# Performance work log

Measured on AMD Instinct MI355X. Metric: run time of the kernel, lower is better.

Reference implementation:

```python
import jax, jax.numpy as jnp
import numpy as np

N, E, C, H, L, G, K, NC = 50000, 500000, 256, 128, 4, 64, 8, 2
EPS_MSG = 1e-7  # GENConv message eps
EPS_BN = 1e-5   # BatchNorm eps


def setup_inputs() -> dict:
    key = jax.random.key(0)
    ks = jax.random.split(key, 32)
    def nrm(k, shape, scale):
        return jax.random.normal(k, shape, dtype=jnp.float32) * scale
    sC = 1.0 / np.sqrt(C).astype(np.float32)
    sH = 1.0 / np.sqrt(H).astype(np.float32)
    s2H = 1.0 / np.sqrt(2 * H).astype(np.float32)
    return dict(
        x=nrm(ks[0], (N, C), 1.0),
        edge_index=jax.random.randint(ks[1], (2, E), 0, N, dtype=jnp.int32),
        edge_attr=jax.random.uniform(ks[2], (E, 1), dtype=jnp.float32),
        batch=jnp.sort(jax.random.randint(ks[3], (N,), 0, G, dtype=jnp.int32)),
        clinical=nrm(ks[4], (G, K), 1.0),
        lin_src_w=nrm(ks[5], (C, H), sC), lin_src_b=nrm(ks[6], (H,), 0.01),
        lin_dst_w=nrm(ks[7], (C, H), sC), lin_dst_b=nrm(ks[8], (H,), 0.01),
        edge_w=nrm(ks[9], (L, 1, H), 1.0), edge_b=nrm(ks[10], (L, H), 0.01),
        t=0.1 + 0.01 * jax.random.normal(ks[11], (L,), dtype=jnp.float32),
        mlp_w1=nrm(ks[12], (L, H, 2 * H), sH), mlp_b1=nrm(ks[13], (L, 2 * H), 0.01),
        mlp_bn_g=1.0 + nrm(ks[14], (L, 2 * H), 0.1), mlp_bn_b=nrm(ks[15], (L, 2 * H), 0.1),
        mlp_bn_m=nrm(ks[16], (L, 2 * H), 0.1),
        mlp_bn_v=1.0 + jax.random.uniform(ks[17], (L, 2 * H), dtype=jnp.float32),
        mlp_w2=nrm(ks[18], (L, 2 * H, H), s2H), mlp_b2=nrm(ks[19], (L, H), 0.01),
        norm_g=1.0 + nrm(ks[20], (L, H), 0.1), norm_b=nrm(ks[21], (L, H), 0.1),
        norm_m=nrm(ks[22], (L, H), 0.1),
        norm_v=1.0 + jax.random.uniform(ks[23], (L, H), dtype=jnp.float32),
        cls_w=nrm(ks[24], (H + K, NC), 1.0 / np.sqrt(H + K).astype(np.float32)),
        cls_b=nrm(ks[25], (NC,), 0.01),
    )


def _bn(h, g, b, m, v):
    # eval-mode BatchNorm with running stats
    return g * (h - m) * jax.lax.rsqrt(v + EPS_BN) + b


def reference(x, edge_index, edge_attr, batch, clinical,
              lin_src_w, lin_src_b, lin_dst_w, lin_dst_b,
              edge_w, edge_b, t,
              mlp_w1, mlp_b1, mlp_bn_g, mlp_bn_b, mlp_bn_m, mlp_bn_v,
              mlp_w2, mlp_b2, norm_g, norm_b, norm_m, norm_v,
              cls_w, cls_b):
    n = x.shape[0]
    g_count = clinical.shape[0]
    src, dst = edge_index[0], edge_index[1]
    n_layers = t.shape[0]

    def genconv(xs, xd, l):
        # xs: source features feeding messages [N,H]; xd: dst skip features [N,H]
        e = edge_attr @ edge_w[l] + edge_b[l]               # [E,H]
        msg = jax.nn.relu(xs[src] + e) + EPS_MSG            # [E,H]
        z = msg * t[l]
        zmax = jax.ops.segment_max(z, dst, num_segments=n)  # [N,H]
        zmax = jnp.where(jnp.isfinite(zmax), zmax, 0.0)
        ez = jnp.exp(z - zmax[dst])
        denom = jax.ops.segment_sum(ez, dst, num_segments=n)
        agg = jax.ops.segment_sum(msg * ez, dst, num_segments=n) / jnp.maximum(denom, 1e-16)
        out = agg + xd
        # internal MLP [H, 2H, H]: Linear -> BN -> ReLU -> Linear
        hmid = jax.nn.relu(_bn(out @ mlp_w1[l] + mlp_b1[l],
                               mlp_bn_g[l], mlp_bn_b[l], mlp_bn_m[l], mlp_bn_v[l]))
        return hmid @ mlp_w2[l] + mlp_b2[l]

    # layer 0: conv only (per DeepGCN.forward); lin_src / lin_dst project C -> H
    xs0 = x @ lin_src_w + lin_src_b
    xd0 = x @ lin_dst_w + lin_dst_b
    h = genconv(xs0, xd0, 0)

    # layers 1..L-1: res+ block (norm -> act -> conv, residual add); dropout = identity (eval)
    for l in range(1, n_layers):
        r = jax.nn.relu(_bn(h, norm_g[l], norm_b[l], norm_m[l], norm_v[l]))
        h = h + genconv(r, r, l)

    # final norm/act from layer 0
    h = jax.nn.relu(_bn(h, norm_g[0], norm_b[0], norm_m[0], norm_v[0]))

    # global mean pool over graphs
    cnt = jax.ops.segment_sum(jnp.ones((n,), h.dtype), batch, num_segments=g_count)
    pooled = jax.ops.segment_sum(h, batch, num_segments=g_count) / jnp.maximum(cnt, 1.0)[:, None]

    z = jnp.concatenate([pooled, clinical], axis=1)
    return z @ cls_w + cls_b  # [G, num_classes]; squeeze is a no-op for G>1, NC=2
```

## Files before the change

### kernel.cpp

```cpp
#include <hip/hip_runtime.h>
#include <math.h>

#define Nn 50000
#define MPAD 50048
#define Ee 500000
#define Cc 256
#define Hh 128
#define Ll 4
#define Gg 64
#define Kk 8
#define NCc 2

#define NB 196

typedef __attribute__((ext_vector_type(8))) short short8;
typedef __attribute__((ext_vector_type(4))) float f32x4;
typedef __attribute__((ext_vector_type(2))) float f32x2;

__device__ __forceinline__ unsigned short f2bf(float f) {
    union { float f; unsigned int u; } v;
    v.f = f;
    unsigned int u = v.u;
    return (unsigned short)((u + 0x7FFFu + ((u >> 16) & 1u)) >> 16);
}
__device__ __forceinline__ float bf2f(unsigned short s) {
    union { float f; unsigned int u; } v;
    v.u = ((unsigned int)s) << 16;
    return v.f;
}
__device__ __forceinline__ float bf2f_lo(unsigned int u) {
    union { float f; unsigned int u; } v;
    v.u = u << 16;
    return v.f;
}
__device__ __forceinline__ float bf2f_hi(unsigned int u) {
    union { float f; unsigned int u; } v;
    v.u = u & 0xffff0000u;
    return v.f;
}


__global__ void hist_kernel(const int* __restrict__ dst, int* __restrict__ deg) {
    int e = blockIdx.x * 256 + threadIdx.x;
    if (e < Ee) atomicAdd(&deg[dst[e]], 1);
}

__global__ __launch_bounds__(256) void bsum_kernel(const int* __restrict__ deg,
                                                   int* __restrict__ bsum) {
    __shared__ int ws[4];
    int t = threadIdx.x;
    int i = blockIdx.x * 256 + t;
    int v = (i < Nn) ? deg[i] : 0;
#pragma unroll
    for (int o = 32; o; o >>= 1) v += __shfl_down(v, o, 64);
    if ((t & 63) == 0) ws[t >> 6] = v;
    __syncthreads();
    if (t == 0) bsum[blockIdx.x] = ws[0] + ws[1] + ws[2] + ws[3];
}

__global__ __launch_bounds__(256) void bscan_kernel(const int* __restrict__ bsum,
                                                    int* __restrict__ boff,
                                                    int* __restrict__ off) {
    __shared__ int sc[256];
    int t = threadIdx.x;
    int v = (t < NB) ? bsum[t] : 0;
    sc[t] = v;
    __syncthreads();
    for (int o = 1; o < 256; o <<= 1) {
        int u = (t >= o) ? sc[t - o] : 0;
        __syncthreads();
        sc[t] += u;
        __syncthreads();
    }
    if (t < NB) boff[t] = sc[t] - v;
    if (t == NB - 1) off[Nn] = sc[t];
}

__global__ __launch_bounds__(256) void offsets_kernel(const int* __restrict__ deg,
                                                      const int* __restrict__ boff,
                                                      int* __restrict__ off,
                                                      int* __restrict__ pos) {
    __shared__ int sc[256];
    int t = threadIdx.x;
    int i = blockIdx.x * 256 + t;
    int v = (i < Nn) ? deg[i] : 0;
    sc[t] = v;
    __syncthreads();
    for (int o = 1; o < 256; o <<= 1) {
        int u = (t >= o) ? sc[t - o] : 0;
        __syncthreads();
        sc[t] += u;
        __syncthreads();
    }
    int excl = sc[t] - v + boff[blockIdx.x];
    if (i < Nn) {
        off[i] = excl;
        pos[i] = excl;
    }
}

__global__ void scatter_kernel(const int* __restrict__ src, const int* __restrict__ dst,
                               const float* __restrict__ attr, int* __restrict__ pos,
                               int2* __restrict__ sedge) {
    int e = blockIdx.x * 256 + threadIdx.x;
    if (e < Ee) {
        int d = dst[e];
        int p = atomicAdd(&pos[d], 1);
        sedge[p] = make_int2(src[e], __float_as_int(attr[e]));
    }
}


__global__ void wconv_kernel(const float* __restrict__ lin_src_w,
                             const float* __restrict__ lin_dst_w,
                             const float* __restrict__ mlp_w1,
                             const float* __restrict__ mlp_w2,
                             unsigned short* __restrict__ wt) {
    int idx = blockIdx.x * 256 + threadIdx.x;
    if (idx >= 327680) return;
    float val;
    if (idx < 65536) {
        int n = idx >> 8, k = idx & 255;
        val = (n < 128) ? lin_src_w[k * 128 + n] : lin_dst_w[k * 128 + (n - 128)];
    } else if (idx < 196608) {
        int r = idx - 65536;
        int l = r >> 15, e = r & 32767;
        int n = e >> 7, k = e & 127;
        val = mlp_w1[(size_t)l * 32768 + k * 256 + n];
    } else {
        int r = idx - 196608;
        int l = r >> 15, e = r & 32767;
        int n = e >> 8, k = e & 255;
        val = mlp_w2[(size_t)l * 32768 + k * 128 + n];
    }
    wt[idx] = f2bf(val);
}


__global__ __launch_bounds__(256) void xconv_kernel(const float* __restrict__ x,
                                                    unsigned short* __restrict__ xbf) {
    int idx = blockIdx.x * 256 + threadIdx.x;
    if (idx >= (Nn * Cc) / 8) return;
    const float4* p = (const float4*)(x) + (size_t)idx * 2;
    float4 v0 = p[0], v1 = p[1];
    unsigned short t[8];
    t[0] = f2bf(v0.x); t[1] = f2bf(v0.y); t[2] = f2bf(v0.z); t[3] = f2bf(v0.w);
    t[4] = f2bf(v1.x); t[5] = f2bf(v1.y); t[6] = f2bf(v1.z); t[7] = f2bf(v1.w);
    *(short8*)(xbf + (size_t)idx * 8) = *(short8*)t;
}

#define GLOAD16(gp, lp)                                                                       \
    __builtin_amdgcn_global_load_lds(                                                         \
        (const __attribute__((address_space(1))) unsigned int*)(gp),                          \
        (__attribute__((address_space(3))) unsigned int*)(lp), 16, 0, 0)


__global__ __launch_bounds__(256) void proj_kernel(
    const unsigned short* __restrict__ A, const unsigned short* __restrict__ Bt,
    const float* __restrict__ bias, const float* __restrict__ bias2,
    unsigned short* __restrict__ Cout) {
    __shared__ __align__(16) unsigned short SH[24576];
    int tid = threadIdx.x;
    int wave = tid >> 6, lane = tid & 63;
    int wr = wave >> 1, wc = wave & 1;
    int lrow = lane & 15, quad = lane >> 4;
    int m0 = blockIdx.y * 128, n0 = blockIdx.x * 128;
    const int K = 256;

    const unsigned short* ag0 = A + (size_t)(m0 + (tid >> 2)) * K + (tid & 3) * 8;
    const unsigned short* ag1 = A + (size_t)(m0 + 64 + (tid >> 2)) * K + (tid & 3) * 8;
    const unsigned short* bg0 = Bt + (size_t)(n0 + (tid >> 2)) * K + (tid & 3) * 8;
    const unsigned short* bg1 = Bt + (size_t)(n0 + 64 + (tid >> 2)) * K + (tid & 3) * 8;

    f32x4 acc[4][4];
#pragma unroll
    for (int i = 0; i < 4; i++)
#pragma unroll
        for (int j = 0; j < 4; j++) acc[i][j] = (f32x4){0.f, 0.f, 0.f, 0.f};

    auto stage = [&](int buf, int koff) {
        GLOAD16(ag0 + koff, SH + buf * 4096 + wave * 512);
        GLOAD16(ag1 + koff, SH + buf * 4096 + 2048 + wave * 512);
        GLOAD16(bg0 + koff, SH + 12288 + buf * 4096 + wave * 512);
        GLOAD16(bg1 + koff, SH + 12288 + buf * 4096 + 2048 + wave * 512);
    };

    const int ntiles = 8;
    stage(0, 0);
    stage(1, 32);
    for (int t = 0; t < ntiles; ++t) {
        if (t + 1 < ntiles) {
            asm volatile("s_waitcnt vmcnt(4)\n\ts_barrier" ::: "memory");
        } else {
            asm volatile("s_waitcnt vmcnt(0)\n\ts_barrier" ::: "memory");
        }
        if (t + 2 < ntiles) stage((t + 2) % 3, (t + 2) * 32);
        int cur = t % 3;
        const unsigned short* As = SH + cur * 4096;
        const unsigned short* Bs = SH + 12288 + cur * 4096;
        short8 af[4], bfr[4];
#pragma unroll
        for (int mt = 0; mt < 4; mt++)
            af[mt] = *(const short8*)&As[(wr * 64 + mt * 16 + lrow) * 32 + quad * 8];
#pragma unroll
        for (int nf = 0; nf < 4; nf++)
            bfr[nf] = *(const short8*)&Bs[(wc * 64 + nf * 16 + lrow) * 32 + quad * 8];
#pragma unroll
        for (int mt = 0; mt < 4; mt++)
#pragma unroll
            for (int nf = 0; nf < 4; nf++)
                acc[mt][nf] = __builtin_amdgcn_mfma_f32_16x16x32_bf16(af[mt], bfr[nf],
                                                                     acc[mt][nf], 0, 0, 0);
    }

    __syncthreads();
    unsigned short* Cl = SH;
#pragma unroll
    for (int nf = 0; nf < 4; nf++) {
        int gc = n0 + wc * 64 + nf * 16 + lrow;
        float bs = (gc >= 128) ? bias2[gc - 128] : bias[gc];
        int col = wc * 64 + nf * 16 + lrow;
#pragma unroll
        for (int mt = 0; mt < 4; mt++)
#pragma unroll
            for (int r = 0; r < 4; r++)
                Cl[(wr * 64 + mt * 16 + quad * 4 + r) * 128 + col] = f2bf(acc[mt][nf][r] + bs);
    }
    __syncthreads();
#pragma unroll
    for (int p = 0; p < 8; p++) {
        int vid = p * 256 + tid;
        int row = vid >> 4, cg = (vid & 15) * 8;
        short8 v = *(const short8*)&Cl[row * 128 + cg];
        *(short8*)(Cout + (size_t)(m0 + row) * 256 + n0 + cg) = v;
    }
}


__global__ __launch_bounds__(256) void mlp_kernel(
    const unsigned short* __restrict__ A,
    const unsigned short* __restrict__ W1,
    const unsigned short* __restrict__ W2,
    const float* __restrict__ b1, const float* __restrict__ bn_g,
    const float* __restrict__ bn_b, const float* __restrict__ bn_m,
    const float* __restrict__ bn_v, const float* __restrict__ b2,
    const float* __restrict__ pn_g, const float* __restrict__ pn_b,
    const float* __restrict__ pn_m, const float* __restrict__ pn_v,
    float* __restrict__ hbuf, unsigned short* __restrict__ rbuf, int rmw) {
    __shared__ __align__(16) unsigned short S[20480];
    __shared__ __align__(16) unsigned short Hm[64 * 264];

    int tid = threadIdx.x;
    int wave = tid >> 6, lane = tid & 63;
    int lrow = lane & 15, quad = lane >> 4;
    int m0 = blockIdx.x * 64;

    const unsigned short* ag = A + (size_t)(m0 + (tid >> 2)) * 128 + (tid & 3) * 8;
    const unsigned short* bg = W1 + (size_t)(tid >> 2) * 128 + (tid & 3) * 8;

    f32x4 acc1[4][4];
#pragma unroll
    for (int i = 0; i < 4; i++)
#pragma unroll
        for (int j = 0; j < 4; j++) acc1[i][j] = (f32x4){0.f, 0.f, 0.f, 0.f};

    auto stage1 = [&](int buf, int k0) {
        GLOAD16(ag + k0, S + buf * 2048 + wave * 512);
#pragma unroll
        for (int c = 0; c < 4; c++)
            GLOAD16(bg + (size_t)c * 64 * 128 + k0,
                    S + 4096 + buf * 8192 + c * 2048 + wave * 512);
    };

    stage1(0, 0);
    __syncthreads();
    for (int t = 0; t < 4; ++t) {
        if (t + 1 < 4) stage1((t + 1) & 1, (t + 1) * 32);
        int cur = t & 1;
        const unsigned short* A1s = S + cur * 2048;
        const unsigned short* B1s = S + 4096 + cur * 8192;
        short8 af[4], bfr[4];
#pragma unroll
        for (int mt = 0; mt < 4; mt++)
            af[mt] = *(const short8*)&A1s[(mt * 16 + lrow) * 32 + quad * 8];
#pragma unroll
        for (int nf = 0; nf < 4; nf++)
            bfr[nf] = *(const short8*)&B1s[(wave * 64 + nf * 16 + lrow) * 32 + quad * 8];
#pragma unroll
        for (int mt = 0; mt < 4; mt++)
#pragma unroll
            for (int nf = 0; nf < 4; nf++)
                acc1[mt][nf] = __builtin_amdgcn_mfma_f32_16x16x32_bf16(af[mt], bfr[nf],
                                                                      acc1[mt][nf], 0, 0, 0);
        __syncthreads();
    }

#pragma unroll
    for (int nf = 0; nf < 4; nf++) {
        int gc = wave * 64 + nf * 16 + lrow;
        float bs = b1[gc];
        float g = bn_g[gc], bb = bn_b[gc], mm = bn_m[gc];
        float inv = rsqrtf(bn_v[gc] + 1e-5f);
#pragma unroll
        for (int mt = 0; mt < 4; mt++)
#pragma unroll
            for (int r = 0; r < 4; r++) {
                float v = acc1[mt][nf][r] + bs;
                v = fmaxf(g * (v - mm) * inv + bb, 0.f);
                Hm[(mt * 16 + quad * 4 + r) * 264 + gc] = f2bf(v);
            }
    }
    __syncthreads();

    const unsigned short* b2g0 = W2 + (size_t)(tid >> 2) * 256 + (tid & 3) * 8;
    const unsigned short* b2g1 = W2 + (size_t)(64 + (tid >> 2)) * 256 + (tid & 3) * 8;

    f32x4 acc2[4][2];
#pragma unroll
    for (int i = 0; i < 4; i++)
#pragma unroll
        for (int j = 0; j < 2; j++) acc2[i][j] = (f32x4){0.f, 0.f, 0.f, 0.f};

    auto stage2 = [&](int buf, int k0) {
        GLOAD16(b2g0 + k0, S + buf * 4096 + wave * 512);
        GLOAD16(b2g1 + k0, S + buf * 4096 + 2048 + wave * 512);
    };

    stage2(0, 0);
    __syncthreads();
    for (int t = 0; t < 8; ++t) {
        if (t + 1 < 8) stage2((t + 1) & 1, (t + 1) * 32);
        int cur = t & 1;
        const unsigned short* B2s = S + cur * 4096;
        short8 af[4], bfr[2];
#pragma unroll
        for (int mt = 0; mt < 4; mt++)
            af[mt] = *(const short8*)&Hm[(mt * 16 + lrow) * 264 + t * 32 + quad * 8];
#pragma unroll
        for (int nf = 0; nf < 2; nf++)
            bfr[nf] = *(const short8*)&B2s[(wave * 32 + nf * 16 + lrow) * 32 + quad * 8];
#pragma unroll
        for (int mt = 0; mt < 4; mt++)
#pragma unroll
            for (int nf = 0; nf < 2; nf++)
                acc2[mt][nf] = __builtin_amdgcn_mfma_f32_16x16x32_bf16(af[mt], bfr[nf],
                                                                      acc2[mt][nf], 0, 0, 0);
        __syncthreads();
    }

    float* C2 = (float*)S;
#pragma unroll
    for (int nf = 0; nf < 2; nf++) {
        int gc = wave * 32 + nf * 16 + lrow;
        float bs = b2[gc];
#pragma unroll
        for (int mt = 0; mt < 4; mt++)
#pragma unroll
            for (int r = 0; r < 4; r++)
                C2[(mt * 16 + quad * 4 + r) * 128 + gc] = acc2[mt][nf][r] + bs;
    }
    __syncthreads();
#pragma unroll
    for (int p = 0; p < 8; p++) {
        int vid = p * 256 + tid;
        int row = vid >> 5, c4 = (vid & 31) * 4;
        f32x4 v = *(const f32x4*)&C2[row * 128 + c4];
        float* hp = hbuf + (size_t)(m0 + row) * 128 + c4;
        if (rmw) v += *(const f32x4*)hp;
        *(f32x4*)hp = v;
        if (pn_g) {
            f32x4 pg = *(const f32x4*)&pn_g[c4];
            f32x4 pb = *(const f32x4*)&pn_b[c4];
            f32x4 pm = *(const f32x4*)&pn_m[c4];
            f32x4 pv = *(const f32x4*)&pn_v[c4];
            float r0 = fmaxf(pg[0] * (v[0] - pm[0]) * rsqrtf(pv[0] + 1e-5f) + pb[0], 0.f);
            float r1 = fmaxf(pg[1] * (v[1] - pm[1]) * rsqrtf(pv[1] + 1e-5f) + pb[1], 0.f);
            float r2 = fmaxf(pg[2] * (v[2] - pm[2]) * rsqrtf(pv[2] + 1e-5f) + pb[2], 0.f);
            float r3 = fmaxf(pg[3] * (v[3] - pm[3]) * rsqrtf(pv[3] + 1e-5f) + pb[3], 0.f);
            unsigned int w0 = (unsigned int)f2bf(r0) | ((unsigned int)f2bf(r1) << 16);
            unsigned int w1 = (unsigned int)f2bf(r2) | ((unsigned int)f2bf(r3) << 16);
            uint2 pk = make_uint2(w0, w1);
            *(uint2*)(rbuf + (size_t)(m0 + row) * 128 + c4) = pk;
        }
    }
}


template <int XSS>
__global__ __launch_bounds__(256) void agg_kernel(
    const unsigned short* __restrict__ xs,
    const unsigned short* __restrict__ xd, int xds,
    const int2* __restrict__ sedge, const int* __restrict__ off,
    const float* __restrict__ ew, const float* __restrict__ eb,
    const float* __restrict__ tptr, unsigned short* __restrict__ outb) {
    int wave = threadIdx.x >> 6;
    int lane = threadIdx.x & 63;
    int d = blockIdx.x * 4 + wave;
    int s0 = __builtin_amdgcn_readfirstlane(off[d]);
    int s1 = __builtin_amdgcn_readfirstlane(off[d + 1]);
    int f0 = lane * 2;
    unsigned int ud = *(const unsigned int*)(xd + (size_t)d * xds + f0);
    f32x2 wv = *(const f32x2*)(ew + f0);
    f32x2 bv = *(const f32x2*)(eb + f0);
    float c = tptr[0] * 1.44269504088896f;
    const f32x2 zz = {0.f, 0.f};
    f32x2 den = {0.f, 0.f}, num = {0.f, 0.f};

#define EDGE2(u, av)                                                \
    {                                                               \
        f32x2 xv = {bf2f_lo(u), bf2f_hi(u)};                        \
        f32x2 m = __builtin_elementwise_max(xv + bv + (av)*wv, zz); \
        f32x2 e;                                                    \
        e.x = __builtin_amdgcn_exp2f(m.x * c);                      \
        e.y = __builtin_amdgcn_exp2f(m.y * c);                      \
        den += e;                                                   \
        num += m * e;                                               \
    }
#define EDGE2M(u, av, mk)                                           \
    {                                                               \
        f32x2 xv = {bf2f_lo(u), bf2f_hi(u)};                        \
        f32x2 m = __builtin_elementwise_max(xv + bv + (av)*wv, zz); \
        f32x2 e;                                                    \
        e.x = __builtin_amdgcn_exp2f(m.x * c) * (mk);               \
        e.y = __builtin_amdgcn_exp2f(m.y * c) * (mk);               \
        den += e;                                                   \
        num += m * e;                                               \
    }

    int j = s0;
    for (; j + 8 <= s1; j += 8) {
        int4 q0 = *(const int4*)(sedge + j);
        int4 q1 = *(const int4*)(sedge + j + 2);
        int4 q2 = *(const int4*)(sedge + j + 4);
        int4 q3 = *(const int4*)(sedge + j + 6);
        int i0 = __builtin_amdgcn_readfirstlane(q0.x);
        int i1 = __builtin_amdgcn_readfirstlane(q0.z);
        int i2 = __builtin_amdgcn_readfirstlane(q1.x);
        int i3 = __builtin_amdgcn_readfirstlane(q1.z);
        int i4 = __builtin_amdgcn_readfirstlane(q2.x);
        int i5 = __builtin_amdgcn_readfirstlane(q2.z);
        int i6 = __builtin_amdgcn_readfirstlane(q3.x);
        int i7 = __builtin_amdgcn_readfirstlane(q3.z);
        float a0 = __int_as_float(__builtin_amdgcn_readfirstlane(q0.y));
        float a1 = __int_as_float(__builtin_amdgcn_readfirstlane(q0.w));
        float a2 = __int_as_float(__builtin_amdgcn_readfirstlane(q1.y));
        float a3 = __int_as_float(__builtin_amdgcn_readfirstlane(q1.w));
        float a4 = __int_as_float(__builtin_amdgcn_readfirstlane(q2.y));
        float a5 = __int_as_float(__builtin_amdgcn_readfirstlane(q2.w));
        float a6 = __int_as_float(__builtin_amdgcn_readfirstlane(q3.y));
        float a7 = __int_as_float(__builtin_amdgcn_readfirstlane(q3.w));
        unsigned int u0 = *(const unsigned int*)(xs + (size_t)i0 * XSS + f0);
        unsigned int u1 = *(const unsigned int*)(xs + (size_t)i1 * XSS + f0);
        unsigned int u2 = *(const unsigned int*)(xs + (size_t)i2 * XSS + f0);
        unsigned int u3 = *(const unsigned int*)(xs + (size_t)i3 * XSS + f0);
        unsigned int u4 = *(const unsigned int*)(xs + (size_t)i4 * XSS + f0);
        unsigned int u5 = *(const unsigned int*)(xs + (size_t)i5 * XSS + f0);
        unsigned int u6 = *(const unsigned int*)(xs + (size_t)i6 * XSS + f0);
        unsigned int u7 = *(const unsigned int*)(xs + (size_t)i7 * XSS + f0);
        EDGE2(u0, a0)
        EDGE2(u1, a1)
        EDGE2(u2, a2)
        EDGE2(u3, a3)
        EDGE2(u4, a4)
        EDGE2(u5, a5)
        EDGE2(u6, a6)
        EDGE2(u7, a7)
    }
    if (j < s1) {
        int last = s1 - 1;
        int ii[8];
        float aa[8], mk[8];
#pragma unroll
        for (int k = 0; k < 8; k++) {
            int jj = j + k;
            int cl = (jj < s1) ? jj : last;
            int2 p = sedge[cl];
            ii[k] = __builtin_amdgcn_readfirstlane(p.x);
            aa[k] = __int_as_float(__builtin_amdgcn_readfirstlane(p.y));
            mk[k] = (jj < s1) ? 1.f : 0.f;
        }
        unsigned int uu[8];
#pragma unroll
        for (int k = 0; k < 8; k++)
            uu[k] = *(const unsigned int*)(xs + (size_t)ii[k] * XSS + f0);
#pragma unroll
        for (int k = 0; k < 8; k++) EDGE2M(uu[k], aa[k], mk[k])
    }
#undef EDGE2
#undef EDGE2M
    float a0 = (s1 > s0) ? (num.x / den.x + 1e-7f) : 0.f;
    float a1 = (s1 > s0) ? (num.y / den.y + 1e-7f) : 0.f;
    unsigned int lo = f2bf(a0 + bf2f_lo(ud));
    unsigned int hi = f2bf(a1 + bf2f_hi(ud));
    *(unsigned int*)(outb + (size_t)d * Hh + f0) = lo | (hi << 16);
}


#define PCHUNK 100

__global__ __launch_bounds__(128) void pool_kernel(
    const float* __restrict__ h, const int* __restrict__ batch,
    const float* __restrict__ g, const float* __restrict__ b,
    const float* __restrict__ m, const float* __restrict__ v,
    float* __restrict__ pooled, float* __restrict__ cnt) {
    int hh = threadIdx.x;
    int i0 = blockIdx.x * PCHUNK;
    int i1 = min(i0 + PCHUNK, Nn);
    if (i0 >= Nn) return;
    float gg = g[hh], bb = b[hh], mm = m[hh], inv = rsqrtf(v[hh] + 1e-5f);
    int cur = batch[i0];
    float sum = 0.f, c = 0.f;
    for (int i = i0; i < i1; i++) {
        int gid = batch[i];
        float val = fmaxf(gg * (h[(size_t)i * Hh + hh] - mm) * inv + bb, 0.f);
        if (gid != cur) {
            atomicAdd(&pooled[(size_t)cur * Hh + hh], sum);
            if (hh == 0) atomicAdd(&cnt[cur], c);
            cur = gid;
            sum = 0.f;
            c = 0.f;
        }
        sum += val;
        c += 1.f;
    }
    atomicAdd(&pooled[(size_t)cur * Hh + hh], sum);
    if (hh == 0) atomicAdd(&cnt[cur], c);
}


__global__ __launch_bounds__(128) void cls_kernel(const float* __restrict__ pooled,
                                                  const float* __restrict__ cnt,
                                                  const float* __restrict__ clinical,
                                                  const float* __restrict__ w,
                                                  const float* __restrict__ bias,
                                                  float* __restrict__ out) {
    int t = threadIdx.x;
    int g = t >> 1, c = t & 1;
    float inv = 1.f / fmaxf(cnt[g], 1.f);
    float s = bias[c];
    for (int j = 0; j < Hh; j++) s += pooled[g * Hh + j] * inv * w[j * NCc + c];
    for (int k = 0; k < Kk; k++) s += clinical[g * Kk + k] * w[(Hh + k) * NCc + c];
    out[g * NCc + c] = s;
}


extern "C" void kernel_launch(void* const* d_in, const int* in_sizes, int n_in,
                              void* d_out, int out_size, void* d_ws, size_t ws_size,
                              hipStream_t stream) {
    const float* x = (const float*)d_in[0];
    const int* eidx = (const int*)d_in[1];
    const float* eattr = (const float*)d_in[2];
    const int* batch = (const int*)d_in[3];
    const float* clinical = (const float*)d_in[4];
    const float* lin_src_w = (const float*)d_in[5];
    const float* lin_src_b = (const float*)d_in[6];
    const float* lin_dst_w = (const float*)d_in[7];
    const float* lin_dst_b = (const float*)d_in[8];
    const float* edge_w = (const float*)d_in[9];
    const float* edge_b = (const float*)d_in[10];
    const float* tt = (const float*)d_in[11];
    const float* mlp_w1 = (const float*)d_in[12];
    const float* mlp_b1 = (const float*)d_in[13];
    const float* bn_g = (const float*)d_in[14];
    const float* bn_b = (const float*)d_in[15];
    const float* bn_m = (const float*)d_in[16];
    const float* bn_v = (const float*)d_in[17];
    const float* mlp_w2 = (const float*)d_in[18];
    const float* mlp_b2 = (const float*)d_in[19];
    const float* norm_g = (const float*)d_in[20];
    const float* norm_b = (const float*)d_in[21];
    const float* norm_m = (const float*)d_in[22];
    const float* norm_v = (const float*)d_in[23];
    const float* cls_w = (const float*)d_in[24];
    const float* cls_b = (const float*)d_in[25];
    float* out = (float*)d_out;

    const int* src = eidx;
    const int* dst = eidx + Ee;

    char* ws = (char*)d_ws;
    size_t off_b = 0;
    auto alloc = [&](size_t bytes) -> void* {
        void* p = ws + off_b;
        off_b += (bytes + 255) & ~(size_t)255;
        return p;
    };
    unsigned short* xsd = (unsigned short*)alloc((size_t)MPAD * 256 * 2);
    unsigned short* rbuf = (unsigned short*)alloc((size_t)MPAD * Hh * 2);
    unsigned short* aggout = (unsigned short*)alloc((size_t)MPAD * Hh * 2);
    unsigned short* xbf = (unsigned short*)alloc((size_t)MPAD * 256 * 2);
    float* hbuf = (float*)alloc((size_t)MPAD * Hh * 4);
    int* deg = (int*)alloc((Nn + 1) * 4);
    int* offp = (int*)alloc((Nn + 1) * 4);
    int* pos = (int*)alloc((size_t)Nn * 4);
    int* bsum = (int*)alloc(NB * 4);
    int* boff = (int*)alloc(NB * 4);
    int2* sedge = (int2*)alloc((size_t)Ee * 8);
    float* pooled = (float*)alloc((size_t)Gg * Hh * 4);
    float* cntb = (float*)alloc(Gg * 4);
    unsigned short* wt = (unsigned short*)alloc((size_t)327680 * 2);

    hipMemsetAsync(deg, 0, (Nn + 1) * 4, stream);
    hipMemsetAsync(pooled, 0, (size_t)Gg * Hh * 4, stream);
    hipMemsetAsync(cntb, 0, Gg * 4, stream);

    hist_kernel<<<(Ee + 255) / 256, 256, 0, stream>>>(dst, deg);
    bsum_kernel<<<NB, 256, 0, stream>>>(deg, bsum);
    bscan_kernel<<<1, 256, 0, stream>>>(bsum, boff, offp);
    offsets_kernel<<<NB, 256, 0, stream>>>(deg, boff, offp, pos);
    scatter_kernel<<<(Ee + 255) / 256, 256, 0, stream>>>(src, dst, eattr, pos, sedge);
    wconv_kernel<<<1280, 256, 0, stream>>>(lin_src_w, lin_dst_w, mlp_w1, mlp_w2, wt);
    xconv_kernel<<<(Nn * Cc / 8 + 255) / 256, 256, 0, stream>>>(x, xbf);

    const unsigned short* wt_proj = wt;
    const unsigned short* wt_w1 = wt + 65536;
    const unsigned short* wt_w2 = wt + 196608;

    dim3 gproj(2, MPAD / 128);
    proj_kernel<<<gproj, 256, 0, stream>>>(xbf, wt_proj, lin_src_b, lin_dst_b, xsd);

    for (int l = 0; l < Ll; l++) {
        if (l == 0) {
            agg_kernel<256><<<Nn / 4, 256, 0, stream>>>(xsd, xsd + 128, 256, sedge, offp,
                                                        edge_w + l * Hh, edge_b + l * Hh,
                                                        tt + l, aggout);
        } else {
            agg_kernel<128><<<Nn / 4, 256, 0, stream>>>(rbuf, rbuf, Hh, sedge, offp,
                                                        edge_w + l * Hh, edge_b + l * Hh,
                                                        tt + l, aggout);
        }
        const float* png = (l < Ll - 1) ? (norm_g + (l + 1) * Hh) : nullptr;
        const float* pnb = (l < Ll - 1) ? (norm_b + (l + 1) * Hh) : nullptr;
        const float* pnm = (l < Ll - 1) ? (norm_m + (l + 1) * Hh) : nullptr;
        const float* pnv = (l < Ll - 1) ? (norm_v + (l + 1) * Hh) : nullptr;
        mlp_kernel<<<MPAD / 64, 256, 0, stream>>>(
            aggout, wt_w1 + (size_t)l * 32768, wt_w2 + (size_t)l * 32768,
            mlp_b1 + l * 2 * Hh, bn_g + l * 2 * Hh, bn_b + l * 2 * Hh,
            bn_m + l * 2 * Hh, bn_v + l * 2 * Hh, mlp_b2 + l * Hh,
            png, pnb, pnm, pnv, hbuf, rbuf, (l == 0) ? 0 : 1);
    }

    pool_kernel<<<(Nn + PCHUNK - 1) / PCHUNK, 128, 0, stream>>>(hbuf, batch, norm_g, norm_b,
                                                                norm_m, norm_v, pooled, cntb);
    cls_kernel<<<1, 128, 0, stream>>>(pooled, cntb, clinical, cls_w, cls_b, out);
}
```

Baseline: 483.7 us.

## Fuse final norm and mean-pool into last MLP; process two nodes per wave in aggregation

The final BatchNorm+ReLU and global mean pool are moved into the epilogue of the last-layer MLP kernel. Each block accumulates up to four graph slots in shared memory with atomics, then flushes them to global memory, so the final hbuf write and the separate pool kernel's re-read go away. The aggregation kernel now handles two destination nodes per wave with interleaved gathers to raise memory-level parallelism, at the cost of more registers and divergent tail handling. The pooling assumes at most four graphs per 64-row block, with overflow clamped into slot 3, which is a correctness risk if batch ids skip more widely.

```diff
diff --git a/kernel.cpp b/kernel.cpp
--- a/kernel.cpp
+++ b/kernel.cpp
@@ -16,6 +16,8 @@
 typedef __attribute__((ext_vector_type(8))) short short8;
 typedef __attribute__((ext_vector_type(4))) float f32x4;
 typedef __attribute__((ext_vector_type(2))) float f32x2;
+
+#define RFL __builtin_amdgcn_readfirstlane
 
 __device__ __forceinline__ unsigned short f2bf(float f) {
     union { float f; unsigned int u; } v;
@@ -246,7 +248,9 @@
     const float* __restrict__ bn_v, const float* __restrict__ b2,
     const float* __restrict__ pn_g, const float* __restrict__ pn_b,
     const float* __restrict__ pn_m, const float* __restrict__ pn_v,
-    float* __restrict__ hbuf, unsigned short* __restrict__ rbuf, int rmw) {
+    float* __restrict__ hbuf, unsigned short* __restrict__ rbuf,
+    const int* __restrict__ batch, float* __restrict__ pooled,
+    float* __restrict__ cnt, int rmw, int dopool) {
     __shared__ __align__(16) unsigned short S[20480];
     __shared__ __align__(16) unsigned short Hm[64 * 264];
 
@@ -349,6 +353,7 @@
     }
 
     float* C2 = (float*)S;
+    float* PS = (float*)S + 8192;
 #pragma unroll
     for (int nf = 0; nf < 2; nf++) {
         int gc = wave * 32 + nf * 16 + lrow;
@@ -359,7 +364,12 @@
             for (int r = 0; r < 4; r++)
                 C2[(mt * 16 + quad * 4 + r) * 128 + gc] = acc2[mt][nf][r] + bs;
     }
-    __syncthreads();
+    if (dopool) {
+        for (int f = tid; f < 532; f += 256) PS[f] = 0.f;
+    }
+    __syncthreads();
+
+    int gfirst = dopool ? RFL(batch[m0]) : 0;
 #pragma unroll
     for (int p = 0; p < 8; p++) {
         int vid = p * 256 + tid;
@@ -367,8 +377,23 @@
         f32x4 v = *(const f32x4*)&C2[row * 128 + c4];
         float* hp = hbuf + (size_t)(m0 + row) * 128 + c4;
         if (rmw) v += *(const f32x4*)hp;
-        *(f32x4*)hp = v;
-        if (pn_g) {
+        if (!dopool) {
+            *(f32x4*)hp = v;
+            if (pn_g) {
+                f32x4 pg = *(const f32x4*)&pn_g[c4];
+                f32x4 pb = *(const f32x4*)&pn_b[c4];
+                f32x4 pm = *(const f32x4*)&pn_m[c4];
+                f32x4 pv = *(const f32x4*)&pn_v[c4];
+                float r0 = fmaxf(pg[0] * (v[0] - pm[0]) * rsqrtf(pv[0] + 1e-5f) + pb[0], 0.f);
+                float r1 = fmaxf(pg[1] * (v[1] - pm[1]) * rsqrtf(pv[1] + 1e-5f) + pb[1], 0.f);
+                float r2 = fmaxf(pg[2] * (v[2] - pm[2]) * rsqrtf(pv[2] + 1e-5f) + pb[2], 0.f);
+                float r3 = fmaxf(pg[3] * (v[3] - pm[3]) * rsqrtf(pv[3] + 1e-5f) + pb[3], 0.f);
+                unsigned int w0 = (unsigned int)f2bf(r0) | ((unsigned int)f2bf(r1) << 16);
+                unsigned int w1 = (unsigned int)f2bf(r2) | ((unsigned int)f2bf(r3) << 16);
+                uint2 pk = make_uint2(w0, w1);
+                *(uint2*)(rbuf + (size_t)(m0 + row) * 128 + c4) = pk;
+            }
+        } else if (m0 + row < Nn) {
             f32x4 pg = *(const f32x4*)&pn_g[c4];
             f32x4 pb = *(const f32x4*)&pn_b[c4];
             f32x4 pm = *(const f32x4*)&pn_m[c4];
@@ -377,11 +402,23 @@
             float r1 = fmaxf(pg[1] * (v[1] - pm[1]) * rsqrtf(pv[1] + 1e-5f) + pb[1], 0.f);
             float r2 = fmaxf(pg[2] * (v[2] - pm[2]) * rsqrtf(pv[2] + 1e-5f) + pb[2], 0.f);
             float r3 = fmaxf(pg[3] * (v[3] - pm[3]) * rsqrtf(pv[3] + 1e-5f) + pb[3], 0.f);
-            unsigned int w0 = (unsigned int)f2bf(r0) | ((unsigned int)f2bf(r1) << 16);
-            unsigned int w1 = (unsigned int)f2bf(r2) | ((unsigned int)f2bf(r3) << 16);
-            uint2 pk = make_uint2(w0, w1);
-            *(uint2*)(rbuf + (size_t)(m0 + row) * 128 + c4) = pk;
+            int slot = min(batch[m0 + row] - gfirst, 3);
+            float* ps = PS + slot * 132 + c4;
+            atomicAdd(ps + 0, r0);
+            atomicAdd(ps + 1, r1);
+            atomicAdd(ps + 2, r2);
+            atomicAdd(ps + 3, r3);
+            if ((vid & 31) == 0) atomicAdd(PS + 528 + slot, 1.f);
         }
+    }
+    if (dopool) {
+        __syncthreads();
+        for (int f = tid; f < 512; f += 256) {
+            int slot = f >> 7, ff = f & 127;
+            int gslot = gfirst + slot;
+            if (gslot < Gg) atomicAdd(&pooled[gslot * 128 + ff], PS[slot * 132 + ff]);
+        }
+        if (tid < 4 && gfirst + tid < Gg) atomicAdd(&cnt[gfirst + tid], PS[528 + tid]);
     }
 }
 
@@ -395,18 +432,21 @@
     const float* __restrict__ tptr, unsigned short* __restrict__ outb) {
     int wave = threadIdx.x >> 6;
     int lane = threadIdx.x & 63;
-    int d = blockIdx.x * 4 + wave;
-    int s0 = __builtin_amdgcn_readfirstlane(off[d]);
-    int s1 = __builtin_amdgcn_readfirstlane(off[d + 1]);
+    int d0 = blockIdx.x * 8 + wave * 2;
+    int d1 = d0 + 1;
     int f0 = lane * 2;
-    unsigned int ud = *(const unsigned int*)(xd + (size_t)d * xds + f0);
+    unsigned int uda = *(const unsigned int*)(xd + (size_t)d0 * xds + f0);
+    unsigned int udb = *(const unsigned int*)(xd + (size_t)d1 * xds + f0);
     f32x2 wv = *(const f32x2*)(ew + f0);
     f32x2 bv = *(const f32x2*)(eb + f0);
     float c = tptr[0] * 1.44269504088896f;
     const f32x2 zz = {0.f, 0.f};
-    f32x2 den = {0.f, 0.f}, num = {0.f, 0.f};
-
-#define EDGE2(u, av)                                                \
+    int s0a = RFL(off[d0]), s1a = RFL(off[d0 + 1]);
+    int s0b = RFL(off[d1]), s1b = RFL(off[d1 + 1]);
+    f32x2 dena = {0.f, 0.f}, numa = {0.f, 0.f};
+    f32x2 denb = {0.f, 0.f}, numb = {0.f, 0.f};
+
+#define EDGE2(u, av, den, num)                                      \
     {                                                               \
         f32x2 xv = {bf2f_lo(u), bf2f_hi(u)};                        \
         f32x2 m = __builtin_elementwise_max(xv + bv + (av)*wv, zz); \
@@ -416,7 +456,7 @@
         den += e;                                                   \
         num += m * e;                                               \
     }
-#define EDGE2M(u, av, mk)                                           \
+#define EDGE2M(u, av, mk, den, num)                                 \
     {                                                               \
         f32x2 xv = {bf2f_lo(u), bf2f_hi(u)};                        \
         f32x2 m = __builtin_elementwise_max(xv + bv + (av)*wv, zz); \
@@ -426,105 +466,103 @@
         den += e;                                                   \
         num += m * e;                                               \
     }
-
-    int j = s0;
-    for (; j + 8 <= s1; j += 8) {
-        int4 q0 = *(const int4*)(sedge + j);
-        int4 q1 = *(const int4*)(sedge + j + 2);
-        int4 q2 = *(const int4*)(sedge + j + 4);
-        int4 q3 = *(const int4*)(sedge + j + 6);
-        int i0 = __builtin_amdgcn_readfirstlane(q0.x);
-        int i1 = __builtin_amdgcn_readfirstlane(q0.z);
-        int i2 = __builtin_amdgcn_readfirstlane(q1.x);
-        int i3 = __builtin_amdgcn_readfirstlane(q1.z);
-        int i4 = __builtin_amdgcn_readfirstlane(q2.x);
-        int i5 = __builtin_amdgcn_readfirstlane(q2.z);
-        int i6 = __builtin_amdgcn_readfirstlane(q3.x);
-        int i7 = __builtin_amdgcn_readfirstlane(q3.z);
-        float a0 = __int_as_float(__builtin_amdgcn_readfirstlane(q0.y));
-        float a1 = __int_as_float(__builtin_amdgcn_readfirstlane(q0.w));
-        float a2 = __int_as_float(__builtin_amdgcn_readfirstlane(q1.y));
-        float a3 = __int_as_float(__builtin_amdgcn_readfirstlane(q1.w));
-        float a4 = __int_as_float(__builtin_amdgcn_readfirstlane(q2.y));
-        float a5 = __int_as_float(__builtin_amdgcn_readfirstlane(q2.w));
-        float a6 = __int_as_float(__builtin_amdgcn_readfirstlane(q3.y));
-        float a7 = __int_as_float(__builtin_amdgcn_readfirstlane(q3.w));
-        unsigned int u0 = *(const unsigned int*)(xs + (size_t)i0 * XSS + f0);
-        unsigned int u1 = *(const unsigned int*)(xs + (size_t)i1 * XSS + f0);
-        unsigned int u2 = *(const unsigned int*)(xs + (size_t)i2 * XSS + f0);
-        unsigned int u3 = *(const unsigned int*)(xs + (size_t)i3 * XSS + f0);
-        unsigned int u4 = *(const unsigned int*)(xs + (size_t)i4 * XSS + f0);
-        unsigned int u5 = *(const unsigned int*)(xs + (size_t)i5 * XSS + f0);
-        unsigned int u6 = *(const unsigned int*)(xs + (size_t)i6 * XSS + f0);
-        unsigned int u7 = *(const unsigned int*)(xs + (size_t)i7 * XSS + f0);
-        EDGE2(u0, a0)
-        EDGE2(u1, a1)
-        EDGE2(u2, a2)
-        EDGE2(u3, a3)
-        EDGE2(u4, a4)
-        EDGE2(u5, a5)
-        EDGE2(u6, a6)
-        EDGE2(u7, a7)
-    }
-    if (j < s1) {
-        int last = s1 - 1;
-        int ii[8];
-        float aa[8], mk[8];
+#define LOADMETA(jv, ii, aa)                                   \
+    {                                                          \
+        int4 q0 = *(const int4*)(sedge + (jv));                \
+        int4 q1 = *(const int4*)(sedge + (jv) + 2);            \
+        int4 q2 = *(const int4*)(sedge + (jv) + 4);            \
+        int4 q3 = *(const int4*)(sedge + (jv) + 6);            \
+        ii[0] = RFL(q0.x); aa[0] = __int_as_float(RFL(q0.y));  \
+        ii[1] = RFL(q0.z); aa[1] = __int_as_float(RFL(q0.w));  \
+        ii[2] = RFL(q1.x); aa[2] = __int_as_float(RFL(q1.y));  \
+        ii[3] = RFL(q1.z); aa[3] = __int_as_float(RFL(q1.w));  \
+        ii[4] = RFL(q2.x); aa[4] = __int_as_float(RFL(q2.y));  \
+        ii[5] = RFL(q2.z); aa[5] = __int_as_float(RFL(q2.w));  \
+        ii[6] = RFL(q3.x); aa[6] = __int_as_float(RFL(q3.y));  \
+        ii[7] = RFL(q3.z); aa[7] = __int_as_float(RFL(q3.w));  \
+    }
+#define GATHER8(ii, uu)                                                          \
+    _Pragma("unroll") for (int k = 0; k < 8; k++) uu[k] =                        \
+        *(const unsigned int*)(xs + (size_t)ii[k] * XSS + f0);
+
+    int ja = s0a, jb = s0b;
+    while (ja + 8 <= s1a && jb + 8 <= s1b) {
+        int ia[8], ib[8];
+        float aa[8], ab[8];
+        LOADMETA(ja, ia, aa)
+        LOADMETA(jb, ib, ab)
+        unsigned int ua[8], ub[8];
+        GATHER8(ia, ua)
+        GATHER8(ib, ub)
+#pragma unroll
+        for (int k = 0; k < 8; k++) EDGE2(ua[k], aa[k], dena, numa)
+#pragma unroll
+        for (int k = 0; k < 8; k++) EDGE2(ub[k], ab[k], denb, numb)
+        ja += 8;
+        jb += 8;
+    }
+    while (ja + 8 <= s1a) {
+        int ia[8];
+        float aa[8];
+        LOADMETA(ja, ia, aa)
+        unsigned int ua[8];
+        GATHER8(ia, ua)
+#pragma unroll
+        for (int k = 0; k < 8; k++) EDGE2(ua[k], aa[k], dena, numa)
+        ja += 8;
+    }
+    while (jb + 8 <= s1b) {
+        int ib[8];
+        float ab[8];
+        LOADMETA(jb, ib, ab)
+        unsigned int ub[8];
+        GATHER8(ib, ub)
+#pragma unroll
+        for (int k = 0; k < 8; k++) EDGE2(ub[k], ab[k], denb, numb)
+        jb += 8;
+    }
+    if (ja < s1a || jb < s1b) {
+        int lasta = (s1a > s0a) ? s1a - 1 : 0;
+        int lastb = (s1b > s0b) ? s1b - 1 : 0;
+        int ia[8], ib[8];
+        float aa[8], ab[8], ma[8], mb[8];
 #pragma unroll
         for (int k = 0; k < 8; k++) {
-            int jj = j + k;
-            int cl = (jj < s1) ? jj : last;
+            int jj = ja + k;
+            int cl = (jj < s1a) ? jj : lasta;
             int2 p = sedge[cl];
-            ii[k] = __builtin_amdgcn_readfirstlane(p.x);
-            aa[k] = __int_as_float(__builtin_amdgcn_readfirstlane(p.y));
-            mk[k] = (jj < s1) ? 1.f : 0.f;
+            ia[k] = RFL(p.x);
+            aa[k] = __int_as_float(RFL(p.y));
+            ma[k] = (jj < s1a) ? 1.f : 0.f;
+            jj = jb + k;
+            cl = (jj < s1b) ? jj : lastb;
+            int2 q = sedge[cl];
+            ib[k] = RFL(q.x);
+            ab[k] = __int_as_float(RFL(q.y));
+            mb[k] = (jj < s1b) ? 1.f : 0.f;
         }
-        unsigned int uu[8];
-#pragma unroll
-        for (int k = 0; k < 8; k++)
-            uu[k] = *(const unsigned int*)(xs + (size_t)ii[k] * XSS + f0);
-#pragma unroll
-        for (int k = 0; k < 8; k++) EDGE2M(uu[k], aa[k], mk[k])
+        unsigned int ua[8], ub[8];
+        GATHER8(ia, ua)
+        GATHER8(ib, ub)
+#pragma unroll
+        for (int k = 0; k < 8; k++) EDGE2M(ua[k], aa[k], ma[k], dena, numa)
+#pragma unroll
+        for (int k = 0; k < 8; k++) EDGE2M(ub[k], ab[k], mb[k], denb, numb)
     }
 #undef EDGE2
 #undef EDGE2M
-    float a0 = (s1 > s0) ? (num.x / den.x + 1e-7f) : 0.f;
-    float a1 = (s1 > s0) ? (num.y / den.y + 1e-7f) : 0.f;
-    unsigned int lo = f2bf(a0 + bf2f_lo(ud));
-    unsigned int hi = f2bf(a1 + bf2f_hi(ud));
-    *(unsigned int*)(outb + (size_t)d * Hh + f0) = lo | (hi << 16);
-}
-
-
-#define PCHUNK 100
-
-__global__ __launch_bounds__(128) void pool_kernel(
-    const float* __restrict__ h, const int* __restrict__ batch,
-    const float* __restrict__ g, const float* __restrict__ b,
-    const float* __restrict__ m, const float* __restrict__ v,
-    float* __restrict__ pooled, float* __restrict__ cnt) {
-    int hh = threadIdx.x;
-    int i0 = blockIdx.x * PCHUNK;
-    int i1 = min(i0 + PCHUNK, Nn);
-    if (i0 >= Nn) return;
-    float gg = g[hh], bb = b[hh], mm = m[hh], inv = rsqrtf(v[hh] + 1e-5f);
-    int cur = batch[i0];
-    float sum = 0.f, c = 0.f;
-    for (int i = i0; i < i1; i++) {
-        int gid = batch[i];
-        float val = fmaxf(gg * (h[(size_t)i * Hh + hh] - mm) * inv + bb, 0.f);
-        if (gid != cur) {
-            atomicAdd(&pooled[(size_t)cur * Hh + hh], sum);
-            if (hh == 0) atomicAdd(&cnt[cur], c);
-            cur = gid;
-            sum = 0.f;
-            c = 0.f;
-        }
-        sum += val;
-        c += 1.f;
-    }
-    atomicAdd(&pooled[(size_t)cur * Hh + hh], sum);
-    if (hh == 0) atomicAdd(&cnt[cur], c);
+#undef LOADMETA
+#undef GATHER8
+    float a0 = (s1a > s0a) ? (numa.x / dena.x + 1e-7f) : 0.f;
+    float a1 = (s1a > s0a) ? (numa.y / dena.y + 1e-7f) : 0.f;
+    float b0 = (s1b > s0b) ? (numb.x / denb.x + 1e-7f) : 0.f;
+    float b1 = (s1b > s0b) ? (numb.y / denb.y + 1e-7f) : 0.f;
+    unsigned int lo = f2bf(a0 + bf2f_lo(uda));
+    unsigned int hi = f2bf(a1 + bf2f_hi(uda));
+    *(unsigned int*)(outb + (size_t)d0 * Hh + f0) = lo | (hi << 16);
+    lo = f2bf(b0 + bf2f_lo(udb));
+    hi = f2bf(b1 + bf2f_hi(udb));
+    *(unsigned int*)(outb + (size_t)d1 * Hh + f0) = lo | (hi << 16);
 }
 
 
@@ -621,26 +659,26 @@
 
     for (int l = 0; l < Ll; l++) {
         if (l == 0) {
-            agg_kernel<256><<<Nn / 4, 256, 0, stream>>>(xsd, xsd + 128, 256, sedge, offp,
+            agg_kernel<256><<<Nn / 8, 256, 0, stream>>>(xsd, xsd + 128, 256, sedge, offp,
                                                         edge_w + l * Hh, edge_b + l * Hh,
                                                         tt + l, aggout);
         } else {
-            agg_kernel<128><<<Nn / 4, 256, 0, stream>>>(rbuf, rbuf, Hh, sedge, offp,
+            agg_kernel<128><<<Nn / 8, 256, 0, stream>>>(rbuf, rbuf, Hh, sedge, offp,
                                                         edge_w + l * Hh, edge_b + l * Hh,
                                                         tt + l, aggout);
         }
-        const float* png = (l < Ll - 1) ? (norm_g + (l + 1) * Hh) : nullptr;
-        const float* pnb = (l < Ll - 1) ? (norm_b + (l + 1) * Hh) : nullptr;
-        const float* pnm = (l < Ll - 1) ? (norm_m + (l + 1) * Hh) : nullptr;
-        const float* pnv = (l < Ll - 1) ? (norm_v + (l + 1) * Hh) : nullptr;
+        int dopool = (l == Ll - 1) ? 1 : 0;
+        const float* png = dopool ? norm_g : (norm_g + (l + 1) * Hh);
+        const float* pnb = dopool ? norm_b : (norm_b + (l + 1) * Hh);
+        const float* pnm = dopool ? norm_m : (norm_m + (l + 1) * Hh);
+        const float* pnv = dopool ? norm_v : (norm_v + (l + 1) * Hh);
         mlp_kernel<<<MPAD / 64, 256, 0, stream>>>(
             aggout, wt_w1 + (size_t)l * 32768, wt_w2 + (size_t)l * 32768,
             mlp_b1 + l * 2 * Hh, bn_g + l * 2 * Hh, bn_b + l * 2 * Hh,
             bn_m + l * 2 * Hh, bn_v + l * 2 * Hh, mlp_b2 + l * Hh,
-            png, pnb, pnm, pnv, hbuf, rbuf, (l == 0) ? 0 : 1);
-    }
-
-    pool_kernel<<<(Nn + PCHUNK - 1) / PCHUNK, 128, 0, stream>>>(hbuf, batch, norm_g, norm_b,
-                                                                norm_m, norm_v, pooled, cntb);
+            png, pnb, pnm, pnv, hbuf, rbuf, batch, pooled, cntb,
+            (l == 0) ? 0 : 1, dopool);
+    }
+
     cls_kernel<<<1, 128, 0, stream>>>(pooled, cntb, clinical, cls_w, cls_b, out);
 }
```

New measurement: 501.9 us. 1.04x slower.
